# Optimization experiments

Measured on AMD Instinct MI355X. Metric: run time of the kernel, lower is better.

Reference implementation:

```python
import jax, jax.numpy as jnp
import numpy as np

DELTA = 0.1
NEG_INF = -1e30


def setup_inputs() -> dict:
    key = jax.random.key(0)
    k1, k2, k3, k4 = jax.random.split(key, 4)
    Bs, Bt, D, C = 8192, 8192, 64, 10
    return {
        "src_feas": jax.random.normal(k1, (Bs, D), dtype=jnp.float32),
        "src_labels": jax.random.randint(k2, (Bs,), 0, C, dtype=jnp.int32),
        "tgt_feas": jax.random.normal(k3, (Bt, D), dtype=jnp.float32),
        "tgt_logits": jax.random.normal(k4, (Bt, C), dtype=jnp.float32),
    }


def reference(src_feas, src_labels, tgt_feas, tgt_logits):
    # The original builds the explicit list of positive pairs (i_tgt, j_src)
    # where tgt sample i is 'confident' (top1-top2 logit gap >= delta) and
    # src_labels[j] == argmax(tgt_logits[i]).  The [P, P] score matrix it
    # forms is s[k, l] = src_feas[j_k] . tgt_feas[i_l], which only depends on
    # (j_k, i_l), so sum(diag(log_softmax(s))) collapses to a weighted
    # logsumexp over the [Bs, Bt] cross-domain score matrix. Same math,
    # fully vectorized, order-invariant.
    Bs = src_feas.shape[0]
    C = tgt_logits.shape[1]

    top2 = jax.lax.top_k(tgt_logits, 2)[0]                  # [Bt, 2]
    conf = (top2[:, 0] - top2[:, 1]) >= DELTA               # [Bt]
    cls = jnp.argmax(tgt_logits, axis=1)                    # [Bt]

    # per-class count of source samples
    counts = jnp.zeros((C,), jnp.float32).at[src_labels].add(1.0)  # [C]
    # w[i] = multiplicity of tgt sample i in the pair list
    w = jnp.where(conf, counts[cls], 0.0)                   # [Bt]

    M = src_feas @ tgt_feas.T                               # [Bs, Bt]
    logw = jnp.where(w > 0, jnp.log(jnp.maximum(w, 1.0)), NEG_INF)
    # L[j] = log sum over all pairs l of exp(M[j, i_l])
    L = jax.scipy.special.logsumexp(M + logw[None, :], axis=1)  # [Bs]

    pair_mask = conf[None, :] & (src_labels[:, None] == cls[None, :])  # [Bs, Bt]
    nce_sum = jnp.sum(jnp.where(pair_mask, M - L[:, None], 0.0))
    P = jnp.sum(w)                                          # total pair count
    nce = nce_sum / (-1.0 * Bs * P)
    return nce
```

## Files before the change

kernel.cpp:

```cpp
#include <hip/hip_runtime.h>
#include <hip/hip_bf16.h>

#define BSZ 8192
#define BTZ 8192
#define DD 64
#define NC 10
#define SHIFT2 20.0f
#define LN2 0.69314718055994531f
#define LOG2E 1.44269504088896341f
#define NEG_BIG -1.0e30f

typedef __attribute__((ext_vector_type(8))) short bf16x8;
typedef __attribute__((ext_vector_type(4))) float f32x4;

#if defined(__has_builtin)
#if __has_builtin(__builtin_amdgcn_exp2f)
#define EXP2(x) __builtin_amdgcn_exp2f(x)
#else
#define EXP2(x) exp2f(x)
#endif
#else
#define EXP2(x) exp2f(x)
#endif

__device__ __forceinline__ unsigned short f2bf_rne(float f) {
    unsigned int u = __float_as_uint(f);
    u += 0x7FFFu + ((u >> 16) & 1u);
    return (unsigned short)(u >> 16);
}

__global__ __launch_bounds__(256) void kAB(const float4* __restrict__ src4,
                                           const float4* __restrict__ tgt4,
                                           const int* __restrict__ labels,
                                           const float* __restrict__ logits,
                                           const float* __restrict__ tgtf,
                                           ushort4* __restrict__ srcb,
                                           ushort4* __restrict__ tgtb,
                                           float* __restrict__ S,
                                           float* __restrict__ colbias,
                                           float* __restrict__ cc_part,
                                           float* __restrict__ counts_g,
                                           float* __restrict__ accs,
                                           int* __restrict__ ctrl,
                                           float* __restrict__ T_part) {
    __shared__ float hist[NC];
    __shared__ float chist[NC];
    __shared__ unsigned char cls_l[256];
    __shared__ float red[4 * 640];

    int t = threadIdx.x;
    int b = blockIdx.x;

    if (b < 512) {
        int tid = b * 256 + t;
        float4 s = src4[tid];
        ushort4 os;
        os.x = f2bf_rne(s.x * LOG2E); os.y = f2bf_rne(s.y * LOG2E);
        os.z = f2bf_rne(s.z * LOG2E); os.w = f2bf_rne(s.w * LOG2E);
        srcb[tid] = os;
        float4 v = tgt4[tid];
        ushort4 ot;
        ot.x = f2bf_rne(v.x); ot.y = f2bf_rne(v.y);
        ot.z = f2bf_rne(v.z); ot.w = f2bf_rne(v.w);
        tgtb[tid] = ot;
        return;
    }

    int lb = b - 512;
    int i = lb * 256 + t;

    if (t < NC) { hist[t] = 0.0f; chist[t] = 0.0f; }
    __syncthreads();

    #pragma unroll
    for (int it = 0; it < 32; ++it) atomicAdd(&hist[labels[it * 256 + t]], 1.0f);

    float m1 = -3.0e38f, m2 = -3.0e38f; int cls = 0;
    #pragma unroll
    for (int c = 0; c < NC; ++c) {
        float v = logits[i * NC + c];
        if (v > m1) { m2 = m1; m1 = v; cls = c; }
        else if (v > m2) { m2 = v; }
    }
    bool conf = (m1 - m2) >= 0.1f;
    __syncthreads();

    float cnt = hist[cls];
    bool live = conf && (cnt > 0.0f);
    colbias[i] = live ? (log2f(cnt) - SHIFT2) : NEG_BIG;
    S[i] = 0.0f;
    cls_l[t] = live ? (unsigned char)cls : (unsigned char)255;
    if (conf) atomicAdd(&chist[cls], 1.0f);
    __syncthreads();

    if (t < NC) cc_part[lb * NC + t] = chist[t];
    if (lb == 0) {
        if (t < NC) counts_g[t] = hist[t];
        if (t < 2) accs[t] = 0.0f;
        if (t < 129) ctrl[t] = 0;
    }

    int w = t >> 6, lane = t & 63;
    float Ta[NC];
    #pragma unroll
    for (int c = 0; c < NC; ++c) Ta[c] = 0.0f;
    int I0 = lb * 256;
    for (int k = 0; k < 64; ++k) {
        int li = w * 64 + k;
        int c = (int)cls_l[li];
        c = __builtin_amdgcn_readfirstlane(c);
        if (c < NC) {
            float v = tgtf[(size_t)(I0 + li) * DD + lane];
            if      (c == 0) Ta[0] += v;
            else if (c == 1) Ta[1] += v;
            else if (c == 2) Ta[2] += v;
            else if (c == 3) Ta[3] += v;
            else if (c == 4) Ta[4] += v;
            else if (c == 5) Ta[5] += v;
            else if (c == 6) Ta[6] += v;
            else if (c == 7) Ta[7] += v;
            else if (c == 8) Ta[8] += v;
            else             Ta[9] += v;
        }
    }
    #pragma unroll
    for (int c = 0; c < NC; ++c) red[w * 640 + c * 64 + lane] = Ta[c];
    __syncthreads();
    for (int idx = t; idx < 640; idx += 256)
        T_part[lb * 640 + idx] =
            red[idx] + red[640 + idx] + red[1280 + idx] + red[1920 + idx];
}

__global__ __launch_bounds__(256) void kCD(const unsigned short* __restrict__ srcb,
                                           const unsigned short* __restrict__ tgtb,
                                           const float* __restrict__ colbias,
                                           const float* __restrict__ srcf,
                                           const int* __restrict__ labels,
                                           const float* __restrict__ cc_part,
                                           const float* __restrict__ counts_g,
                                           const float* __restrict__ T_part,
                                           float* __restrict__ S,
                                           float* __restrict__ accs,
                                           int* __restrict__ ctrl,
                                           float* __restrict__ out) {
    __shared__ float lds[4][64];
    __shared__ float Tl[660];
    __shared__ float t1red[4];
    __shared__ float ccl[NC];
    __shared__ int flag1, flag2;

    int t = threadIdx.x;
    int w = t >> 6;
    int lane = t & 63;
    int l15 = lane & 15;
    int quad = lane >> 4;
    int colchunk = blockIdx.x & 15;
    int rowg = blockIdx.x >> 4;
    int row_base = rowg * 64;

    bf16x8 a[4][2];
    #pragma unroll
    for (int mb = 0; mb < 4; ++mb) {
        const bf16x8* p = (const bf16x8*)(srcb + (size_t)(row_base + mb * 16 + l15) * DD + quad * 8);
        a[mb][0] = p[0];
        a[mb][1] = p[4];
    }

    float rs[4][4];
    #pragma unroll
    for (int mb = 0; mb < 4; ++mb)
        #pragma unroll
        for (int r = 0; r < 4; ++r) rs[mb][r] = 0.0f;

    int col0 = colchunk * 512 + w * 128;
    const bf16x8* q0 = (const bf16x8*)(tgtb + (size_t)(col0 + l15) * DD + quad * 8);
    bf16x8 b0 = q0[0];
    bf16x8 b1 = q0[4];
    float cb2 = colbias[col0 + l15];

    #pragma unroll 2
    for (int ct = 0; ct < 8; ++ct) {
        bf16x8 nb0 = b0, nb1 = b1;
        float ncb2 = cb2;
        if (ct < 7) {
            int cb = col0 + (ct + 1) * 16;
            const bf16x8* qn = (const bf16x8*)(tgtb + (size_t)(cb + l15) * DD + quad * 8);
            nb0 = qn[0];
            nb1 = qn[4];
            ncb2 = colbias[cb + l15];
        }
        #pragma unroll
        for (int mb = 0; mb < 4; ++mb) {
            f32x4 acc = {cb2, cb2, cb2, cb2};
            acc = __builtin_amdgcn_mfma_f32_16x16x32_bf16(a[mb][0], b0, acc, 0, 0, 0);
            acc = __builtin_amdgcn_mfma_f32_16x16x32_bf16(a[mb][1], b1, acc, 0, 0, 0);
            #pragma unroll
            for (int r = 0; r < 4; ++r) rs[mb][r] += EXP2(acc[r]);
        }
        b0 = nb0; b1 = nb1; cb2 = ncb2;
    }

    #pragma unroll
    for (int mb = 0; mb < 4; ++mb) {
        #pragma unroll
        for (int r = 0; r < 4; ++r) {
            float v = rs[mb][r];
            v += __shfl_xor(v, 1);
            v += __shfl_xor(v, 2);
            v += __shfl_xor(v, 4);
            v += __shfl_xor(v, 8);
            if (l15 == 0) lds[w][mb * 16 + quad * 4 + r] = v;
        }
    }
    __syncthreads();
    if (t < 64)
        atomicAdd(&S[row_base + t], lds[0][t] + lds[1][t] + lds[2][t] + lds[3][t]);

    if (colchunk == 0) {
        for (int idx = t; idx < 640; idx += 256) {
            float sm = 0.0f;
            #pragma unroll
            for (int p = 0; p < 32; ++p) sm += T_part[p * 640 + idx];
            Tl[(idx >> 6) * 66 + (idx & 63)] = sm;
        }
        __syncthreads();
        int r = t >> 2, dq = t & 3;
        int lab = labels[row_base + r];
        const float4* sp = (const float4*)(srcf + (size_t)(row_base + r) * DD + dq * 16);
        float part = 0.0f;
        #pragma unroll
        for (int j4 = 0; j4 < 4; ++j4) {
            float4 sv = sp[j4];
            int tb = lab * 66 + dq * 16 + j4 * 4;
            part += sv.x * Tl[tb] + sv.y * Tl[tb + 1] + sv.z * Tl[tb + 2] + sv.w * Tl[tb + 3];
        }
        #pragma unroll
        for (int m = 1; m < 64; m <<= 1) part += __shfl_xor(part, m);
        if (lane == 0) t1red[w] = part;
        __syncthreads();
        if (t == 0) atomicAdd(&accs[1], t1red[0] + t1red[1] + t1red[2] + t1red[3]);
    }

    __syncthreads();
    if (t == 0) { int old = atomicAdd(&ctrl[rowg], 1); flag1 = (old == 15) ? 1 : 0; }
    __syncthreads();
    if (!flag1) return;

    if (t < NC) {
        float s = 0.0f;
        #pragma unroll
        for (int p = 0; p < 32; ++p) s += cc_part[p * NC + t];
        ccl[t] = s;
    }
    __syncthreads();
    float val = 0.0f;
    if (t < 64) {
        float s = __hip_atomic_load(&S[row_base + t], __ATOMIC_RELAXED, __HIP_MEMORY_SCOPE_AGENT);
        float L = (log2f(s) + SHIFT2) * LN2;
        val = ccl[labels[row_base + t]] * L;
    }
    if (w == 0) {
        #pragma unroll
        for (int m = 1; m < 64; m <<= 1) val += __shfl_xor(val, m);
        if (t == 0) atomicAdd(&accs[0], val);
    }
    if (t == 0) {
        asm volatile("s_waitcnt vmcnt(0)" ::: "memory");
        int o2 = atomicAdd(&ctrl[128], 1);
        flag2 = (o2 == 127) ? 1 : 0;
    }
    __syncthreads();
    if (flag2 && t == 0) {
        float tl  = __hip_atomic_load(&accs[0], __ATOMIC_RELAXED, __HIP_MEMORY_SCOPE_AGENT);
        float t1v = __hip_atomic_load(&accs[1], __ATOMIC_RELAXED, __HIP_MEMORY_SCOPE_AGENT);
        float P = 0.0f;
        #pragma unroll
        for (int c = 0; c < NC; ++c) P += counts_g[c] * ccl[c];
        out[0] = (t1v - tl) / (-(float)BSZ * P);
    }
}

extern "C" void kernel_launch(void* const* d_in, const int* in_sizes, int n_in,
                              void* d_out, int out_size, void* d_ws, size_t ws_size,
                              hipStream_t stream) {
    const float* src    = (const float*)d_in[0];
    const int*   labels = (const int*)d_in[1];
    const float* tgt    = (const float*)d_in[2];
    const float* logits = (const float*)d_in[3];

    char* ws = (char*)d_ws;
    float* S        = (float*)(ws + 0);
    float* colbias  = (float*)(ws + 32768);
    float* cc_part  = (float*)(ws + 65536);
    float* counts_g = (float*)(ws + 66816);
    float* accs     = (float*)(ws + 66856);
    int*   ctrl     = (int*)(ws + 66864);
    float* T_part   = (float*)(ws + 67584);
    unsigned short* srcb = (unsigned short*)(ws + 163840);
    unsigned short* tgtb = (unsigned short*)(ws + 163840 + 1048576);

    kAB<<<544, 256, 0, stream>>>((const float4*)src, (const float4*)tgt, labels, logits, tgt,
                                 (ushort4*)srcb, (ushort4*)tgtb,
                                 S, colbias, cc_part, counts_g, accs, ctrl, T_part);
    kCD<<<2048, 256, 0, stream>>>(srcb, tgtb, colbias, src, labels,
                                  cc_part, counts_g, T_part, S, accs, ctrl, (float*)d_out);
}
```

Measured before the change: 134.0 us.

## Compute positive-pair term via per-class source/target sums and pipeline tile loads

The positive-pair dot-product term is now computed as the sum over classes of dot(U_c, T_c), where U_c is the per-class source feature sum and T_c the per-class confident target feature sum. Both sums are built in kAB, whose stats blocks now each handle 1024 rows, so only 8 stats blocks are launched instead of 32. This drops the per-row source pass that the colchunk-0 blocks of kCD used to run, and the final block reduces the small partial arrays instead. The target-feature accumulation now batches loads into registers with lane-broadcast class ids, and the kCD column loop is manually triple-buffered. The trade-off is fewer, longer stats blocks in kAB, which may lengthen its tail.

Measured after the change: 193.3 us. +44.2%, slower.

```diff
diff --git a/kernel.cpp b/kernel.cpp
--- a/kernel.cpp
+++ b/kernel.cpp
@@ -23,17 +23,39 @@
 #define EXP2(x) exp2f(x)
 #endif
 
+#define MFMA16(A, B, C) __builtin_amdgcn_mfma_f32_16x16x32_bf16(A, B, C, 0, 0, 0)
+
 __device__ __forceinline__ unsigned short f2bf_rne(float f) {
     unsigned int u = __float_as_uint(f);
     u += 0x7FFFu + ((u >> 16) & 1u);
     return (unsigned short)(u >> 16);
 }
 
+#define ACC10(A, c, v) {                      \
+    if      ((c) == 0) A[0] += (v);           \
+    else if ((c) == 1) A[1] += (v);           \
+    else if ((c) == 2) A[2] += (v);           \
+    else if ((c) == 3) A[3] += (v);           \
+    else if ((c) == 4) A[4] += (v);           \
+    else if ((c) == 5) A[5] += (v);           \
+    else if ((c) == 6) A[6] += (v);           \
+    else if ((c) == 7) A[7] += (v);           \
+    else if ((c) == 8) A[8] += (v);           \
+    else if ((c) == 9) A[9] += (v); }
+
+#define LD8(buf, g) { _Pragma("unroll")       \
+    for (int kk = 0; kk < 8; ++kk) buf[kk] = rowp[(size_t)((((g) * 8) + kk) * 64)]; }
+#define AC8(buf, g, A) { _Pragma("unroll")    \
+    for (int kk = 0; kk < 8; ++kk) {          \
+        int c_ = __builtin_amdgcn_readlane(myc, (g) * 8 + kk);  \
+        ACC10(A, c_, buf[kk]); } }
+
 __global__ __launch_bounds__(256) void kAB(const float4* __restrict__ src4,
                                            const float4* __restrict__ tgt4,
                                            const int* __restrict__ labels,
                                            const float* __restrict__ logits,
                                            const float* __restrict__ tgtf,
+                                           const float* __restrict__ srcf,
                                            ushort4* __restrict__ srcb,
                                            ushort4* __restrict__ tgtb,
                                            float* __restrict__ S,
@@ -42,10 +64,11 @@
                                            float* __restrict__ counts_g,
                                            float* __restrict__ accs,
                                            int* __restrict__ ctrl,
+                                           float* __restrict__ U_part,
                                            float* __restrict__ T_part) {
     __shared__ float hist[NC];
     __shared__ float chist[NC];
-    __shared__ unsigned char cls_l[256];
+    __shared__ unsigned char clsl[1024];
     __shared__ float red[4 * 640];
 
     int t = threadIdx.x;
@@ -67,7 +90,7 @@
     }
 
     int lb = b - 512;
-    int i = lb * 256 + t;
+    int base = lb * 1024;
 
     if (t < NC) { hist[t] = 0.0f; chist[t] = 0.0f; }
     __syncthreads();
@@ -75,22 +98,32 @@
     #pragma unroll
     for (int it = 0; it < 32; ++it) atomicAdd(&hist[labels[it * 256 + t]], 1.0f);
 
-    float m1 = -3.0e38f, m2 = -3.0e38f; int cls = 0;
-    #pragma unroll
-    for (int c = 0; c < NC; ++c) {
-        float v = logits[i * NC + c];
-        if (v > m1) { m2 = m1; m1 = v; cls = c; }
-        else if (v > m2) { m2 = v; }
-    }
-    bool conf = (m1 - m2) >= 0.1f;
-    __syncthreads();
-
-    float cnt = hist[cls];
-    bool live = conf && (cnt > 0.0f);
-    colbias[i] = live ? (log2f(cnt) - SHIFT2) : NEG_BIG;
-    S[i] = 0.0f;
-    cls_l[t] = live ? (unsigned char)cls : (unsigned char)255;
-    if (conf) atomicAdd(&chist[cls], 1.0f);
+    int cls4[4]; int conf4[4];
+    #pragma unroll
+    for (int r = 0; r < 4; ++r) {
+        int i = base + r * 256 + t;
+        float m1 = -3.0e38f, m2 = -3.0e38f; int cls = 0;
+        #pragma unroll
+        for (int c = 0; c < NC; ++c) {
+            float v = logits[i * NC + c];
+            if (v > m1) { m2 = m1; m1 = v; cls = c; }
+            else if (v > m2) { m2 = v; }
+        }
+        cls4[r] = cls;
+        conf4[r] = (m1 - m2) >= 0.1f;
+    }
+    __syncthreads();
+
+    #pragma unroll
+    for (int r = 0; r < 4; ++r) {
+        int i = base + r * 256 + t;
+        float cnt = hist[cls4[r]];
+        int live = conf4[r] && (cnt > 0.0f);
+        colbias[i] = live ? (log2f(cnt) - SHIFT2) : NEG_BIG;
+        S[i] = 0.0f;
+        clsl[r * 256 + t] = live ? (unsigned char)cls4[r] : (unsigned char)255;
+        if (conf4[r]) atomicAdd(&chist[cls4[r]], 1.0f);
+    }
     __syncthreads();
 
     if (t < NC) cc_part[lb * NC + t] = chist[t];
@@ -101,27 +134,25 @@
     }
 
     int w = t >> 6, lane = t & 63;
+
     float Ta[NC];
     #pragma unroll
     for (int c = 0; c < NC; ++c) Ta[c] = 0.0f;
-    int I0 = lb * 256;
-    for (int k = 0; k < 64; ++k) {
-        int li = w * 64 + k;
-        int c = (int)cls_l[li];
-        c = __builtin_amdgcn_readfirstlane(c);
-        if (c < NC) {
-            float v = tgtf[(size_t)(I0 + li) * DD + lane];
-            if      (c == 0) Ta[0] += v;
-            else if (c == 1) Ta[1] += v;
-            else if (c == 2) Ta[2] += v;
-            else if (c == 3) Ta[3] += v;
-            else if (c == 4) Ta[4] += v;
-            else if (c == 5) Ta[5] += v;
-            else if (c == 6) Ta[6] += v;
-            else if (c == 7) Ta[7] += v;
-            else if (c == 8) Ta[8] += v;
-            else             Ta[9] += v;
-        }
+    #pragma unroll
+    for (int ch = 0; ch < 4; ++ch) {
+        int rowb = base + w * 256 + ch * 64;
+        int myc = (int)clsl[w * 256 + ch * 64 + lane];
+        const float* rowp = tgtf + (size_t)rowb * DD + lane;
+        float pA[8], pB[8];
+        LD8(pA, 0) LD8(pB, 1)
+        AC8(pA, 0, Ta) LD8(pA, 2)
+        AC8(pB, 1, Ta) LD8(pB, 3)
+        AC8(pA, 2, Ta) LD8(pA, 4)
+        AC8(pB, 3, Ta) LD8(pB, 5)
+        AC8(pA, 4, Ta) LD8(pA, 6)
+        AC8(pB, 5, Ta) LD8(pB, 7)
+        AC8(pA, 6, Ta)
+        AC8(pB, 7, Ta)
     }
     #pragma unroll
     for (int c = 0; c < NC; ++c) red[w * 640 + c * 64 + lane] = Ta[c];
@@ -129,22 +160,60 @@
     for (int idx = t; idx < 640; idx += 256)
         T_part[lb * 640 + idx] =
             red[idx] + red[640 + idx] + red[1280 + idx] + red[1920 + idx];
+    __syncthreads();
+
+    float Ua[NC];
+    #pragma unroll
+    for (int c = 0; c < NC; ++c) Ua[c] = 0.0f;
+    #pragma unroll
+    for (int ch = 0; ch < 4; ++ch) {
+        int rowb = base + w * 256 + ch * 64;
+        int myc = labels[rowb + lane];
+        const float* rowp = srcf + (size_t)rowb * DD + lane;
+        float pA[8], pB[8];
+        LD8(pA, 0) LD8(pB, 1)
+        AC8(pA, 0, Ua) LD8(pA, 2)
+        AC8(pB, 1, Ua) LD8(pB, 3)
+        AC8(pA, 2, Ua) LD8(pA, 4)
+        AC8(pB, 3, Ua) LD8(pB, 5)
+        AC8(pA, 4, Ua) LD8(pA, 6)
+        AC8(pB, 5, Ua) LD8(pB, 7)
+        AC8(pA, 6, Ua)
+        AC8(pB, 7, Ua)
+    }
+    #pragma unroll
+    for (int c = 0; c < NC; ++c) red[w * 640 + c * 64 + lane] = Ua[c];
+    __syncthreads();
+    for (int idx = t; idx < 640; idx += 256)
+        U_part[lb * 640 + idx] =
+            red[idx] + red[640 + idx] + red[1280 + idx] + red[1920 + idx];
 }
+
+#define LOADT(bx0, bx1, cbx, ctv) {                                            \
+    int cb_ = col0 + (ctv) * 16;                                               \
+    const bf16x8* q_ = (const bf16x8*)(tgtb + (size_t)(cb_ + l15) * DD + quad * 8); \
+    bx0 = q_[0]; bx1 = q_[4]; cbx = colbias[cb_ + l15]; }
+#define COMPT(bx0, bx1, cbx) { _Pragma("unroll")                               \
+    for (int mb = 0; mb < 4; ++mb) {                                           \
+        f32x4 acc = {cbx, cbx, cbx, cbx};                                      \
+        acc = MFMA16(a[mb][0], bx0, acc);                                      \
+        acc = MFMA16(a[mb][1], bx1, acc);                                      \
+        _Pragma("unroll")                                                      \
+        for (int r = 0; r < 4; ++r) rs[mb][r] += EXP2(acc[r]); } }
 
 __global__ __launch_bounds__(256) void kCD(const unsigned short* __restrict__ srcb,
                                            const unsigned short* __restrict__ tgtb,
                                            const float* __restrict__ colbias,
-                                           const float* __restrict__ srcf,
                                            const int* __restrict__ labels,
                                            const float* __restrict__ cc_part,
                                            const float* __restrict__ counts_g,
+                                           const float* __restrict__ U_part,
                                            const float* __restrict__ T_part,
                                            float* __restrict__ S,
                                            float* __restrict__ accs,
                                            int* __restrict__ ctrl,
                                            float* __restrict__ out) {
     __shared__ float lds[4][64];
-    __shared__ float Tl[660];
     __shared__ float t1red[4];
     __shared__ float ccl[NC];
     __shared__ int flag1, flag2;
@@ -173,32 +242,19 @@
         for (int r = 0; r < 4; ++r) rs[mb][r] = 0.0f;
 
     int col0 = colchunk * 512 + w * 128;
-    const bf16x8* q0 = (const bf16x8*)(tgtb + (size_t)(col0 + l15) * DD + quad * 8);
-    bf16x8 b0 = q0[0];
-    bf16x8 b1 = q0[4];
-    float cb2 = colbias[col0 + l15];
-
-    #pragma unroll 2
-    for (int ct = 0; ct < 8; ++ct) {
-        bf16x8 nb0 = b0, nb1 = b1;
-        float ncb2 = cb2;
-        if (ct < 7) {
-            int cb = col0 + (ct + 1) * 16;
-            const bf16x8* qn = (const bf16x8*)(tgtb + (size_t)(cb + l15) * DD + quad * 8);
-            nb0 = qn[0];
-            nb1 = qn[4];
-            ncb2 = colbias[cb + l15];
-        }
-        #pragma unroll
-        for (int mb = 0; mb < 4; ++mb) {
-            f32x4 acc = {cb2, cb2, cb2, cb2};
-            acc = __builtin_amdgcn_mfma_f32_16x16x32_bf16(a[mb][0], b0, acc, 0, 0, 0);
-            acc = __builtin_amdgcn_mfma_f32_16x16x32_bf16(a[mb][1], b1, acc, 0, 0, 0);
-            #pragma unroll
-            for (int r = 0; r < 4; ++r) rs[mb][r] += EXP2(acc[r]);
-        }
-        b0 = nb0; b1 = nb1; cb2 = ncb2;
-    }
+
+    bf16x8 x0, x1, y0, y1, z0, z1;
+    float cx, cy, cz;
+    LOADT(x0, x1, cx, 0)
+    LOADT(y0, y1, cy, 1)
+    LOADT(z0, z1, cz, 2)  COMPT(x0, x1, cx)
+    LOADT(x0, x1, cx, 3)  COMPT(y0, y1, cy)
+    LOADT(y0, y1, cy, 4)  COMPT(z0, z1, cz)
+    LOADT(z0, z1, cz, 5)  COMPT(x0, x1, cx)
+    LOADT(x0, x1, cx, 6)  COMPT(y0, y1, cy)
+    LOADT(y0, y1, cy, 7)  COMPT(z0, z1, cz)
+    COMPT(x0, x1, cx)
+    COMPT(y0, y1, cy)
 
     #pragma unroll
     for (int mb = 0; mb < 4; ++mb) {
@@ -216,31 +272,6 @@
     if (t < 64)
         atomicAdd(&S[row_base + t], lds[0][t] + lds[1][t] + lds[2][t] + lds[3][t]);
 
-    if (colchunk == 0) {
-        for (int idx = t; idx < 640; idx += 256) {
-            float sm = 0.0f;
-            #pragma unroll
-            for (int p = 0; p < 32; ++p) sm += T_part[p * 640 + idx];
-            Tl[(idx >> 6) * 66 + (idx & 63)] = sm;
-        }
-        __syncthreads();
-        int r = t >> 2, dq = t & 3;
-        int lab = labels[row_base + r];
-        const float4* sp = (const float4*)(srcf + (size_t)(row_base + r) * DD + dq * 16);
-        float part = 0.0f;
-        #pragma unroll
-        for (int j4 = 0; j4 < 4; ++j4) {
-            float4 sv = sp[j4];
-            int tb = lab * 66 + dq * 16 + j4 * 4;
-            part += sv.x * Tl[tb] + sv.y * Tl[tb + 1] + sv.z * Tl[tb + 2] + sv.w * Tl[tb + 3];
-        }
-        #pragma unroll
-        for (int m = 1; m < 64; m <<= 1) part += __shfl_xor(part, m);
-        if (lane == 0) t1red[w] = part;
-        __syncthreads();
-        if (t == 0) atomicAdd(&accs[1], t1red[0] + t1red[1] + t1red[2] + t1red[3]);
-    }
-
     __syncthreads();
     if (t == 0) { int old = atomicAdd(&ctrl[rowg], 1); flag1 = (old == 15) ? 1 : 0; }
     __syncthreads();
@@ -249,7 +280,7 @@
     if (t < NC) {
         float s = 0.0f;
         #pragma unroll
-        for (int p = 0; p < 32; ++p) s += cc_part[p * NC + t];
+        for (int p = 0; p < 8; ++p) s += cc_part[p * NC + t];
         ccl[t] = s;
     }
     __syncthreads();
@@ -270,9 +301,29 @@
         flag2 = (o2 == 127) ? 1 : 0;
     }
     __syncthreads();
-    if (flag2 && t == 0) {
+    if (!flag2) return;
+
+    float t1loc = 0.0f;
+    #pragma unroll
+    for (int g = 0; g < 3; ++g) {
+        int idx = g * 256 + t;
+        if (idx < 640) {
+            float u = 0.0f, tv = 0.0f;
+            #pragma unroll
+            for (int p = 0; p < 8; ++p) {
+                u  += U_part[p * 640 + idx];
+                tv += T_part[p * 640 + idx];
+            }
+            t1loc += u * tv;
+        }
+    }
+    #pragma unroll
+    for (int m = 1; m < 64; m <<= 1) t1loc += __shfl_xor(t1loc, m);
+    if (lane == 0) t1red[w] = t1loc;
+    __syncthreads();
+    if (t == 0) {
+        float t1v = t1red[0] + t1red[1] + t1red[2] + t1red[3];
         float tl  = __hip_atomic_load(&accs[0], __ATOMIC_RELAXED, __HIP_MEMORY_SCOPE_AGENT);
-        float t1v = __hip_atomic_load(&accs[1], __ATOMIC_RELAXED, __HIP_MEMORY_SCOPE_AGENT);
         float P = 0.0f;
         #pragma unroll
         for (int c = 0; c < NC; ++c) P += counts_g[c] * ccl[c];
@@ -292,16 +343,18 @@
     float* S        = (float*)(ws + 0);
     float* colbias  = (float*)(ws + 32768);
     float* cc_part  = (float*)(ws + 65536);
-    float* counts_g = (float*)(ws + 66816);
-    float* accs     = (float*)(ws + 66856);
-    int*   ctrl     = (int*)(ws + 66864);
-    float* T_part   = (float*)(ws + 67584);
-    unsigned short* srcb = (unsigned short*)(ws + 163840);
-    unsigned short* tgtb = (unsigned short*)(ws + 163840 + 1048576);
-
-    kAB<<<544, 256, 0, stream>>>((const float4*)src, (const float4*)tgt, labels, logits, tgt,
-                                 (ushort4*)srcb, (ushort4*)tgtb,
-                                 S, colbias, cc_part, counts_g, accs, ctrl, T_part);
-    kCD<<<2048, 256, 0, stream>>>(srcb, tgtb, colbias, src, labels,
-                                  cc_part, counts_g, T_part, S, accs, ctrl, (float*)d_out);
+    float* counts_g = (float*)(ws + 65856);
+    float* accs     = (float*)(ws + 65896);
+    int*   ctrl     = (int*)(ws + 65920);
+    float* U_part   = (float*)(ws + 66560);
+    float* T_part   = (float*)(ws + 87040);
+    unsigned short* srcb = (unsigned short*)(ws + 131072);
+    unsigned short* tgtb = (unsigned short*)(ws + 131072 + 1048576);
+
+    kAB<<<520, 256, 0, stream>>>((const float4*)src, (const float4*)tgt, labels, logits,
+                                 tgt, src, (ushort4*)srcb, (ushort4*)tgtb,
+                                 S, colbias, cc_part, counts_g, accs, ctrl, U_part, T_part);
+    kCD<<<2048, 256, 0, stream>>>(srcb, tgtb, colbias, labels,
+                                  cc_part, counts_g, U_part, T_part,
+                                  S, accs, ctrl, (float*)d_out);
 }
```
